# Kernel optimization log

Hardware: AMD Instinct MI355X
Metric: run time of the kernel (lower is better)

## Reference

```python
import jax, jax.numpy as jnp
import numpy as np

B, C, T = 16, 512, 1024      # batch, in_shape (channels), seq_len
H, D = 8, 64                 # num_heads, head_dim; embed = H*D == C
E = H * D
EPS = 1e-6


def setup_inputs() -> dict:
    key = jax.random.key(0)
    ks = jax.random.split(key, 10)
    s_in = 1.0 / np.sqrt(C)
    s_e = 1.0 / np.sqrt(E)
    return {
        "X": jax.random.normal(ks[0], (B, C, T), jnp.float32),
        "ln_g": jnp.ones((C,), jnp.float32),
        "ln_b": jnp.zeros((C,), jnp.float32),
        "Wq": jax.random.normal(ks[1], (C, E), jnp.float32) * s_in,
        "bq": jnp.zeros((E,), jnp.float32),
        "Wk": jax.random.normal(ks[2], (C, E), jnp.float32) * s_in,
        "bk": jnp.zeros((E,), jnp.float32),
        "Wv": jax.random.normal(ks[3], (C, E), jnp.float32) * s_in,
        "bv": jnp.zeros((E,), jnp.float32),
        "Wo": jax.random.normal(ks[4], (E, C), jnp.float32) * s_e,
        "bo": jnp.zeros((C,), jnp.float32),
    }


def reference(X, ln_g, ln_b, Wq, bq, Wk, bk, Wv, bv, Wo, bo):
    # dimshuffle: (B, C, T) -> (B, T, C)
    x = jnp.transpose(X, (0, 2, 1))
    # pre-norm LayerNorm over last dim, eps=1e-6
    mu = jnp.mean(x, axis=-1, keepdims=True)
    var = jnp.mean(jnp.square(x - mu), axis=-1, keepdims=True)
    xn = (x - mu) * jax.lax.rsqrt(var + EPS) * ln_g + ln_b
    # QKV projections, split into heads: (B, T, H, D)
    q = (xn @ Wq + bq).reshape(B, T, H, D)
    k = (xn @ Wk + bk).reshape(B, T, H, D)
    v = (xn @ Wv + bv).reshape(B, T, H, D)
    # attention: scores (B, H, T, T)
    scores = jnp.einsum("bqhd,bkhd->bhqk", q, k) / np.sqrt(D)
    w = jax.nn.softmax(scores, axis=-1)
    h = jnp.einsum("bhqk,bkhd->bqhd", w, v).reshape(B, T, E)
    out = h @ Wo + bo            # output projection (dropout=0 in eval)
    out = x + out                # residual
    return jnp.transpose(out, (0, 2, 1))  # back to (B, C, T)
```

## Files before the change

### kernel.cpp

```cpp
#include <hip/hip_runtime.h>
#include <hip/hip_bf16.h>
#include <cstdint>
#include <cstddef>

typedef __attribute__((ext_vector_type(8))) __bf16 bf16x8;
typedef __attribute__((ext_vector_type(4))) float f32x4;
typedef __attribute__((ext_vector_type(16))) float f32x16;
typedef __attribute__((ext_vector_type(4))) unsigned short u16x4;
typedef __attribute__((ext_vector_type(4))) unsigned int u32x4;
typedef unsigned int u32;

#define NB 16
#define NC 512
#define NT 1024
#define NH 8
#define ND 64
#define NE 512

__device__ __forceinline__ void gld16(void* lds, const void* g) {
  __builtin_amdgcn_global_load_lds(
      (const __attribute__((address_space(1))) u32*)g,
      (__attribute__((address_space(3))) u32*)lds, 16, 0, 0);
}

__device__ __forceinline__ unsigned short f2bf(float f) {
  __bf16 h = (__bf16)f;
  return __builtin_bit_cast(unsigned short, h);
}

__device__ __forceinline__ float ex2(float x) {
  float r; asm("v_exp_f32 %0, %1" : "=v"(r) : "v"(x)); return r;
}

__device__ __forceinline__ void pl32swap(u32& a, u32& b) {
  asm("v_permlane32_swap_b32 %0, %1" : "+v"(a), "+v"(b));
}

__global__ __launch_bounds__(256) void wt_convert4(
    const float* __restrict__ Wq, const float* __restrict__ Wk,
    const float* __restrict__ Wv, const float* __restrict__ Wo,
    __bf16* __restrict__ Wtq, __bf16* __restrict__ Wtk,
    __bf16* __restrict__ Wtv, __bf16* __restrict__ Wto)
{
  __shared__ float tile[32][33];
  const int w = blockIdx.y;
  const float* W = (w == 0) ? Wq : (w == 1) ? Wk : (w == 2) ? Wv : Wo;
  __bf16*     Wt = (w == 0) ? Wtq : (w == 1) ? Wtk : (w == 2) ? Wtv : Wto;
  const int bx = blockIdx.x & 15, by = blockIdx.x >> 4;
  const int r0 = by * 32, c0 = bx * 32;
  const int tx = threadIdx.x & 31, ty = threadIdx.x >> 5;
#pragma unroll
  for (int i = 0; i < 4; i++)
    tile[ty + i * 8][tx] = W[(size_t)(r0 + ty + i * 8) * 512 + c0 + tx];
  __syncthreads();
#pragma unroll
  for (int i = 0; i < 4; i++) {
    const int cc = ty + i * 8;
    Wt[(size_t)(c0 + cc) * 512 + r0 + tx] = (__bf16)tile[tx][cc];
  }
}

__global__ __launch_bounds__(256) void ln_kernel(
    const float* __restrict__ X, const float* __restrict__ gam,
    const float* __restrict__ bet, __bf16* __restrict__ xn)
{
  __shared__ float tile[16][513];
  __shared__ float mu_s[16], rs_s[16];
  const int b  = blockIdx.x >> 6;
  const int t0 = (blockIdx.x & 63) << 4;
  const int tid = threadIdx.x;
  const int tl = tid & 15, c0 = tid >> 4;
  const float* Xb = X + (size_t)b * NC * NT + t0;
  for (int c = c0; c < NC; c += 16)
    tile[tl][c] = Xb[(size_t)c * NT + tl];
  __syncthreads();
  const int row = tid >> 4, sub = tid & 15;
  float s = 0.f, s2 = 0.f;
  for (int c = sub; c < NC; c += 16) { const float v = tile[row][c]; s += v; s2 += v * v; }
  s += __shfl_xor(s, 1);  s2 += __shfl_xor(s2, 1);
  s += __shfl_xor(s, 2);  s2 += __shfl_xor(s2, 2);
  s += __shfl_xor(s, 4);  s2 += __shfl_xor(s2, 4);
  s += __shfl_xor(s, 8);  s2 += __shfl_xor(s2, 8);
  const float mu   = s * (1.f / NC);
  const float var  = s2 * (1.f / NC) - mu * mu;
  const float rstd = rsqrtf(var + 1e-6f);
  if (sub == 0) { mu_s[row] = mu; rs_s[row] = rstd; }
  __syncthreads();
  __bf16* xo = xn + ((size_t)b * NT + t0) * NC;
  for (int i = tid; i < 16 * NC; i += 256) {
    const int r = i >> 9, c = i & (NC - 1);
    xo[(size_t)r * NC + c] = (__bf16)((tile[r][c] - mu_s[r]) * rs_s[r] * gam[c] + bet[c]);
  }
}

__global__ __launch_bounds__(256) void gemm_qkv(
    const __bf16* __restrict__ A, const __bf16* __restrict__ Wt,
    const float* __restrict__ bq, const float* __restrict__ bk, const float* __restrict__ bv,
    __bf16* __restrict__ qb, __bf16* __restrict__ kb, __bf16* __restrict__ vtb)
{
  __shared__ __align__(16) __bf16 lA[128 * 64];
  __shared__ __align__(16) __bf16 lB[128 * 64];
  __shared__ float tb[4][16][17];
  const int tid = threadIdx.x;
  const int wv = tid >> 6, lane = tid & 63;
  const int bid = blockIdx.x;
  const int mchunk = bid / 192, rem = bid % 192;
  const int xcd = rem & 7, loc = rem >> 3;
  const int mt = mchunk * 16 + xcd * 2 + (loc / 12);
  const int nt = loc % 12;
  const int m0 = mt << 7, n0 = nt << 7;
  const int fr = lane & 15, kq = lane >> 4;
  const int wr = wv >> 1, wc = wv & 1;
  const int swz = (fr & 7) << 4;

  const int so  = wv * 1024 + lane * 16;
  const int srr = so >> 7;
  const int scb = (so & 127) ^ ((srr & 7) << 4);
  const char* Asrc = (const char*)A  + (size_t)(m0 + srr) * 1024 + scb;
  const char* Bsrc = (const char*)Wt + (size_t)(n0 + srr) * 1024 + scb;

  f32x4 acc[4][4] = {};
  for (int k0 = 0; k0 < 8; k0++) {
#pragma unroll
    for (int is = 0; is < 4; is++) {
      gld16((char*)lA + is * 4096 + wv * 1024, Asrc + k0 * 128 + (size_t)is * 32768);
      gld16((char*)lB + is * 4096 + wv * 1024, Bsrc + k0 * 128 + (size_t)is * 32768);
    }
    __syncthreads();
#pragma unroll
    for (int kk = 0; kk < 2; kk++) {
      bf16x8 af[4], bfr[4];
#pragma unroll
      for (int i = 0; i < 4; i++) {
        af[i]  = *(const bf16x8*)((const char*)lA +
                   (wr * 64 + i * 16 + fr) * 128 + ((kk * 64 + kq * 16) ^ swz));
        bfr[i] = *(const bf16x8*)((const char*)lB +
                   (wc * 64 + i * 16 + fr) * 128 + ((kk * 64 + kq * 16) ^ swz));
      }
#pragma unroll
      for (int i = 0; i < 4; i++)
#pragma unroll
        for (int j = 0; j < 4; j++)
          acc[i][j] = __builtin_amdgcn_mfma_f32_16x16x32_bf16(af[i], bfr[j], acc[i][j], 0, 0, 0);
    }
    __syncthreads();
  }

  const int wsel = n0 >> 9;
  const float* bias = (wsel == 0) ? bq : (wsel == 1) ? bk : bv;
  const float qsc = (wsel == 0) ? 0.18033688011112042f : 1.0f;
  if (wsel < 2) {
#pragma unroll
    for (int i = 0; i < 4; i++) {
#pragma unroll
      for (int j = 0; j < 4; j++) {
        const int ng = (n0 & 511) + wc * 64 + j * 16 + fr;
        const int hh = ng >> 6, dd = ng & 63;
        const float bb = bias[ng];
#pragma unroll
        for (int r = 0; r < 4; r++) {
          const int mg = m0 + wr * 64 + i * 16 + kq * 4 + r;
          const int b = mg >> 10, t = mg & 1023;
          const __bf16 h16 = (__bf16)((acc[i][j][r] + bb) * qsc);
          if (wsel == 0) qb[(((size_t)b * NH + hh) * NT + t) * ND + dd] = h16;
          else           kb[(((size_t)b * NH + hh) * NT + t) * ND + dd] = h16;
        }
      }
    }
  } else {
#pragma unroll
    for (int i = 0; i < 4; i++) {
#pragma unroll
      for (int j = 0; j < 4; j++) {
#pragma unroll
        for (int r = 0; r < 4; r++) tb[wv][kq * 4 + r][fr] = acc[i][j][r];
#pragma unroll
        for (int rr = 0; rr < 4; rr++) {
          const int cloc = kq * 4 + rr;
          const int ng = (n0 & 511) + wc * 64 + j * 16 + cloc;
          const int hh = ng >> 6, dd = ng & 63;
          const int mg = m0 + wr * 64 + i * 16 + fr;
          const int b = mg >> 10, t = mg & 1023;
          vtb[(((size_t)b * NH + hh) * ND + dd) * NT + t] =
              (__bf16)(tb[wv][fr][cloc] + bias[ng]);
        }
      }
    }
  }
}

__global__ __launch_bounds__(128, 2) void attn_kernel(
    const __bf16* __restrict__ qb, const __bf16* __restrict__ kb,
    const __bf16* __restrict__ vtb, __bf16* __restrict__ hb)
{
  __shared__ __align__(16) __bf16 lK[2][4096];
  __shared__ __align__(16) __bf16 lV[2][4096];
  const int tid = threadIdx.x, wv = tid >> 6, lane = tid & 63;
  const int l31 = lane & 31, hi = lane >> 5;
  const int swz = (l31 & 7) << 4;
  const int bid = blockIdx.x;
  const int xcd = bid & 7, idx = bid >> 3;
  const int hbp = xcd * 16 + (idx >> 3);
  const int chunk = idx & 7;
  const int b = hbp >> 3, hh = hbp & 7;
  const int q0 = chunk * 128 + wv * 64;

  const __bf16* Q = qb + ((size_t)b * NH + hh) * NT * ND;
  const char* Kc = (const char*)(kb  + ((size_t)b * NH + hh) * NT * ND);
  const char* Vc = (const char*)(vtb + ((size_t)b * NH + hh) * ND * NT);

  const int so  = wv * 1024 + lane * 16;
  const int srr = so >> 7;
  const int scb = (so & 127) ^ ((srr & 7) << 4);
  const char* Ksrc0 = Kc + (size_t)srr * 128 + scb;
  const char* Vsrc0 = Vc + (size_t)srr * 2048 + scb;

  bf16x8 qf[2][4];
#pragma unroll
  for (int qs = 0; qs < 2; qs++)
#pragma unroll
    for (int ds = 0; ds < 4; ds++)
      qf[qs][ds] = *(const bf16x8*)&Q[(size_t)(q0 + qs * 32 + l31) * ND + ds * 16 + hi * 8];

  float l_run[2] = {0.f, 0.f};
  f32x16 O[2][2] = {};
  const f32x16 zz = {};

  auto stage = [&](int nb, int kt64) {
#pragma unroll
    for (int is = 0; is < 4; is++) {
      gld16((char*)&lK[nb][0] + is * 2048 + wv * 1024,
            Ksrc0 + (size_t)kt64 * 128 + is * 2048);
      gld16((char*)&lV[nb][0] + is * 2048 + wv * 1024,
            Vsrc0 + (size_t)kt64 * 2 + is * 32768);
    }
  };

  stage(0, 0);
  stage(1, 64);

#pragma unroll 1
  for (int ti = 0; ti < 16; ti++) {
    const int cur = ti & 1;
    if (ti < 15) asm volatile("s_waitcnt vmcnt(8)" ::: "memory");
    else         asm volatile("s_waitcnt vmcnt(0)" ::: "memory");
    __builtin_amdgcn_s_barrier();
    __builtin_amdgcn_sched_barrier(0);
    const char* Kb = (const char*)&lK[cur][0];
    const char* Vb = (const char*)&lV[cur][0];

    f32x16 st[2][2];
    __builtin_amdgcn_s_setprio(1);
#pragma unroll
    for (int ks = 0; ks < 2; ks++) {
#pragma unroll
      for (int ds = 0; ds < 4; ds++) {
        const int row = ks * 32 + l31;
        const bf16x8 ka = *(const bf16x8*)
            (Kb + row * 128 + ((ds * 32 + hi * 16) ^ swz));
        if (ds == 0) {
          st[0][ks] = __builtin_amdgcn_mfma_f32_32x32x16_bf16(ka, qf[0][0], zz, 0, 0, 0);
          st[1][ks] = __builtin_amdgcn_mfma_f32_32x32x16_bf16(ka, qf[1][0], zz, 0, 0, 0);
        } else {
          st[0][ks] = __builtin_amdgcn_mfma_f32_32x32x16_bf16(ka, qf[0][ds], st[0][ks], 0, 0, 0);
          st[1][ks] = __builtin_amdgcn_mfma_f32_32x32x16_bf16(ka, qf[1][ds], st[1][ks], 0, 0, 0);
        }
      }
    }
    __builtin_amdgcn_s_setprio(0);

#pragma unroll
    for (int qs = 0; qs < 2; qs++) {
      float rs = 0.f;
      u32 pk[2][4][2];
#pragma unroll
      for (int ks = 0; ks < 2; ks++)
#pragma unroll
        for (int g = 0; g < 4; g++) {
          const float p0 = ex2(st[qs][ks][4 * g + 0]);
          const float p1 = ex2(st[qs][ks][4 * g + 1]);
          const float p2 = ex2(st[qs][ks][4 * g + 2]);
          const float p3 = ex2(st[qs][ks][4 * g + 3]);
          rs += (p0 + p1) + (p2 + p3);
          asm("v_cvt_pk_bf16_f32 %0, %1, %2" : "=v"(pk[ks][g][0]) : "v"(p0), "v"(p1));
          asm("v_cvt_pk_bf16_f32 %0, %1, %2" : "=v"(pk[ks][g][1]) : "v"(p2), "v"(p3));
        }
      l_run[qs] += rs;

      __builtin_amdgcn_s_setprio(1);
#pragma unroll
      for (int s = 0; s < 4; s++) {
        const int t = s >> 1, m = s & 1;
        u32 a0 = pk[t][2 * m][0], b0 = pk[t][2 * m + 1][0];
        u32 a1 = pk[t][2 * m][1], b1 = pk[t][2 * m + 1][1];
        pl32swap(a0, b0);
        pl32swap(a1, b1);
        u32x4 w;
        w[0] = a0; w[1] = a1; w[2] = b0; w[3] = b1;
        const bf16x8 pfrag = __builtin_bit_cast(bf16x8, w);
#pragma unroll
        for (int dsub = 0; dsub < 2; dsub++) {
          const int row = dsub * 32 + l31;
          const bf16x8 vf = *(const bf16x8*)
              (Vb + row * 128 + ((s * 32 + hi * 16) ^ swz));
          O[qs][dsub] = __builtin_amdgcn_mfma_f32_32x32x16_bf16(vf, pfrag, O[qs][dsub], 0, 0, 0);
        }
      }
      __builtin_amdgcn_s_setprio(0);
    }

    __builtin_amdgcn_s_barrier();
    __builtin_amdgcn_sched_barrier(0);
    if (ti + 2 < 16) stage(cur, (ti + 2) * 64);
  }

#pragma unroll
  for (int qs = 0; qs < 2; qs++) {
    const float lt = l_run[qs] + __shfl_xor(l_run[qs], 32);
    const float linv = 1.f / lt;
    const int t = q0 + qs * 32 + l31;
    __bf16* hrow = hb + ((size_t)b * NT + t) * NE + hh * ND;
#pragma unroll
    for (int dsub = 0; dsub < 2; dsub++)
#pragma unroll
      for (int g = 0; g < 4; g++) {
        u16x4 ov;
#pragma unroll
        for (int rr = 0; rr < 4; rr++) ov[rr] = f2bf(O[qs][dsub][4 * g + rr] * linv);
        *(u16x4*)&hrow[dsub * 32 + g * 8 + hi * 4] = ov;
      }
  }
}

__global__ __launch_bounds__(256) void gemm_out(
    const __bf16* __restrict__ A, const __bf16* __restrict__ Wt,
    const float* __restrict__ bo, const float* __restrict__ X,
    float* __restrict__ out)
{
  __shared__ __align__(16) __bf16 lA[128 * 64];
  __shared__ __align__(16) __bf16 lB[128 * 64];
  __shared__ float tb[4][16][17];
  const int tid = threadIdx.x, wv = tid >> 6, lane = tid & 63;
  const int bid = blockIdx.x;
  const int mt = ((bid >> 5) << 3) + (bid & 7);
  const int nt = (bid & 31) >> 3;
  const int m0 = mt << 7, n0 = nt << 7;
  const int fr = lane & 15, kq = lane >> 4;
  const int wr = wv >> 1, wc = wv & 1;
  const int swz = (fr & 7) << 4;

  const int so  = wv * 1024 + lane * 16;
  const int srr = so >> 7;
  const int scb = (so & 127) ^ ((srr & 7) << 4);
  const char* Asrc = (const char*)A  + (size_t)(m0 + srr) * 1024 + scb;
  const char* Bsrc = (const char*)Wt + (size_t)(n0 + srr) * 1024 + scb;

  f32x4 acc[4][4] = {};
  for (int k0 = 0; k0 < 8; k0++) {
#pragma unroll
    for (int is = 0; is < 4; is++) {
      gld16((char*)lA + is * 4096 + wv * 1024, Asrc + k0 * 128 + (size_t)is * 32768);
      gld16((char*)lB + is * 4096 + wv * 1024, Bsrc + k0 * 128 + (size_t)is * 32768);
    }
    __syncthreads();
#pragma unroll
    for (int kk = 0; kk < 2; kk++) {
      bf16x8 af[4], bfr[4];
#pragma unroll
      for (int i = 0; i < 4; i++) {
        af[i]  = *(const bf16x8*)((const char*)lA +
                   (wr * 64 + i * 16 + fr) * 128 + ((kk * 64 + kq * 16) ^ swz));
        bfr[i] = *(const bf16x8*)((const char*)lB +
                   (wc * 64 + i * 16 + fr) * 128 + ((kk * 64 + kq * 16) ^ swz));
      }
#pragma unroll
      for (int i = 0; i < 4; i++)
#pragma unroll
        for (int j = 0; j < 4; j++)
          acc[i][j] = __builtin_amdgcn_mfma_f32_16x16x32_bf16(af[i], bfr[j], acc[i][j], 0, 0, 0);
    }
    __syncthreads();
  }

#pragma unroll
  for (int i = 0; i < 4; i++) {
#pragma unroll
    for (int j = 0; j < 4; j++) {
#pragma unroll
      for (int r = 0; r < 4; r++) tb[wv][kq * 4 + r][fr] = acc[i][j][r];
#pragma unroll
      for (int rr = 0; rr < 4; rr++) {
        const int cloc = kq * 4 + rr;
        const int mg = m0 + wr * 64 + i * 16 + fr;
        const int b = mg >> 10, t = mg & 1023;
        const int c = n0 + wc * 64 + j * 16 + cloc;
        out[((size_t)b * NC + c) * NT + t] =
            tb[wv][fr][cloc] + bo[c] + X[((size_t)b * NC + c) * NT + t];
      }
    }
  }
}

extern "C" void kernel_launch(void* const* d_in, const int* in_sizes, int n_in,
                              void* d_out, int out_size, void* d_ws, size_t ws_size,
                              hipStream_t stream) {
  const float* X   = (const float*)d_in[0];
  const float* lng = (const float*)d_in[1];
  const float* lnb = (const float*)d_in[2];
  const float* Wq  = (const float*)d_in[3];
  const float* bq  = (const float*)d_in[4];
  const float* Wk  = (const float*)d_in[5];
  const float* bk  = (const float*)d_in[6];
  const float* Wv  = (const float*)d_in[7];
  const float* bv  = (const float*)d_in[8];
  const float* Wo  = (const float*)d_in[9];
  const float* bo  = (const float*)d_in[10];
  float* out = (float*)d_out;

  __bf16* wsb   = (__bf16*)d_ws;
  __bf16* Wtqkv = wsb;
  __bf16* Wot   = wsb + 786432;
  __bf16* xn    = wsb + 1048576;
  __bf16* qbuf  = wsb + 9437184;
  __bf16* kbuf  = wsb + 17825792;
  __bf16* vtbuf = wsb + 26214400;
  __bf16* hbuf  = wsb + 34603008;

  wt_convert4<<<dim3(256, 4), 256, 0, stream>>>(
      Wq, Wk, Wv, Wo, Wtqkv, Wtqkv + 262144, Wtqkv + 524288, Wot);
  ln_kernel<<<NB * (NT / 16), 256, 0, stream>>>(X, lng, lnb, xn);
  gemm_qkv<<<128 * 12, 256, 0, stream>>>(xn, Wtqkv, bq, bk, bv, qbuf, kbuf, vtbuf);
  attn_kernel<<<1024, 128, 0, stream>>>(qbuf, kbuf, vtbuf, hbuf);
  gemm_out<<<128 * 4, 256, 0, stream>>>(hbuf, Wot, bo, X, out);
}
```

Baseline: 132.6 us.

## Halve attention tile sizes: 32 queries per wave, 32-key blocks, double grid

```diff
diff --git a/kernel.cpp b/kernel.cpp
--- a/kernel.cpp
+++ b/kernel.cpp
@@ -189,147 +189,144 @@
   }
 }
 
-__global__ __launch_bounds__(128, 2) void attn_kernel(
+__global__ __launch_bounds__(128) void attn_kernel(
     const __bf16* __restrict__ qb, const __bf16* __restrict__ kb,
     const __bf16* __restrict__ vtb, __bf16* __restrict__ hb)
 {
-  __shared__ __align__(16) __bf16 lK[2][4096];
-  __shared__ __align__(16) __bf16 lV[2][4096];
+  __shared__ __align__(16) __bf16 lK[2][2048];
+  __shared__ __align__(16) __bf16 lV[2][2048];
   const int tid = threadIdx.x, wv = tid >> 6, lane = tid & 63;
   const int l31 = lane & 31, hi = lane >> 5;
   const int swz = (l31 & 7) << 4;
   const int bid = blockIdx.x;
   const int xcd = bid & 7, idx = bid >> 3;
-  const int hbp = xcd * 16 + (idx >> 3);
-  const int chunk = idx & 7;
+  const int hbp = xcd * 16 + (idx >> 4);
+  const int chunk = idx & 15;
   const int b = hbp >> 3, hh = hbp & 7;
-  const int q0 = chunk * 128 + wv * 64;
+  const int q0 = chunk * 64 + wv * 32;
 
   const __bf16* Q = qb + ((size_t)b * NH + hh) * NT * ND;
   const char* Kc = (const char*)(kb  + ((size_t)b * NH + hh) * NT * ND);
   const char* Vc = (const char*)(vtb + ((size_t)b * NH + hh) * ND * NT);
 
-  const int so  = wv * 1024 + lane * 16;
-  const int srr = so >> 7;
-  const int scb = (so & 127) ^ ((srr & 7) << 4);
-  const char* Ksrc0 = Kc + (size_t)srr * 128 + scb;
-  const char* Vsrc0 = Vc + (size_t)srr * 2048 + scb;
-
-  bf16x8 qf[2][4];
-#pragma unroll
-  for (int qs = 0; qs < 2; qs++)
-#pragma unroll
-    for (int ds = 0; ds < 4; ds++)
-      qf[qs][ds] = *(const bf16x8*)&Q[(size_t)(q0 + qs * 32 + l31) * ND + ds * 16 + hi * 8];
-
-  float l_run[2] = {0.f, 0.f};
-  f32x16 O[2][2] = {};
+  const char* Ks[2];
+  const char* Vs[2];
+#pragma unroll
+  for (int is = 0; is < 2; is++) {
+    const int o  = wv * 2048 + is * 1024 + lane * 16;
+    const int rr = o >> 7, ob = o & 127;
+    const int kcb = ob ^ ((rr & 7) << 4);
+    Ks[is] = Kc + (size_t)rr * 128 + kcb;
+    const int u = ob ^ ((rr & 7) << 4);
+    const int dsub = u >> 6, tb = u & 63;
+    Vs[is] = Vc + (size_t)(dsub * 32 + rr) * 2048 + tb;
+  }
+
+  bf16x8 qf[4];
+#pragma unroll
+  for (int ds = 0; ds < 4; ds++)
+    qf[ds] = *(const bf16x8*)&Q[(size_t)(q0 + l31) * ND + ds * 16 + hi * 8];
+
+  float l_run = 0.f;
+  f32x16 O[2] = {};
   const f32x16 zz = {};
 
-  auto stage = [&](int nb, int kt64) {
-#pragma unroll
-    for (int is = 0; is < 4; is++) {
-      gld16((char*)&lK[nb][0] + is * 2048 + wv * 1024,
-            Ksrc0 + (size_t)kt64 * 128 + is * 2048);
-      gld16((char*)&lV[nb][0] + is * 2048 + wv * 1024,
-            Vsrc0 + (size_t)kt64 * 2 + is * 32768);
+  auto stage = [&](int nb, int kt32) {
+#pragma unroll
+    for (int is = 0; is < 2; is++) {
+      gld16((char*)&lK[nb][0] + wv * 1024 + is * 512 * 2,
+            Ks[is] + (size_t)kt32 * 128);
+      gld16((char*)&lV[nb][0] + wv * 1024 + is * 512 * 2,
+            Vs[is] + (size_t)kt32 * 2);
     }
   };
 
-  stage(0, 0);
-  stage(1, 64);
+  auto stage2 = [&](int nb, int kt32) {
+#pragma unroll
+    for (int is = 0; is < 2; is++) {
+      gld16((char*)&lK[nb][0] + wv * 2048 + is * 1024,
+            Ks[is] + (size_t)kt32 * 128);
+      gld16((char*)&lV[nb][0] + wv * 2048 + is * 1024,
+            Vs[is] + (size_t)kt32 * 2);
+    }
+  };
+
+  stage2(0, 0);
+  stage2(1, 32);
 
 #pragma unroll 1
-  for (int ti = 0; ti < 16; ti++) {
+  for (int ti = 0; ti < 32; ti++) {
     const int cur = ti & 1;
-    if (ti < 15) asm volatile("s_waitcnt vmcnt(8)" ::: "memory");
+    if (ti < 31) asm volatile("s_waitcnt vmcnt(4)" ::: "memory");
     else         asm volatile("s_waitcnt vmcnt(0)" ::: "memory");
     __builtin_amdgcn_s_barrier();
     __builtin_amdgcn_sched_barrier(0);
     const char* Kb = (const char*)&lK[cur][0];
     const char* Vb = (const char*)&lV[cur][0];
 
-    f32x16 st[2][2];
+    f32x16 st;
     __builtin_amdgcn_s_setprio(1);
 #pragma unroll
-    for (int ks = 0; ks < 2; ks++) {
-#pragma unroll
-      for (int ds = 0; ds < 4; ds++) {
-        const int row = ks * 32 + l31;
-        const bf16x8 ka = *(const bf16x8*)
-            (Kb + row * 128 + ((ds * 32 + hi * 16) ^ swz));
-        if (ds == 0) {
-          st[0][ks] = __builtin_amdgcn_mfma_f32_32x32x16_bf16(ka, qf[0][0], zz, 0, 0, 0);
-          st[1][ks] = __builtin_amdgcn_mfma_f32_32x32x16_bf16(ka, qf[1][0], zz, 0, 0, 0);
-        } else {
-          st[0][ks] = __builtin_amdgcn_mfma_f32_32x32x16_bf16(ka, qf[0][ds], st[0][ks], 0, 0, 0);
-          st[1][ks] = __builtin_amdgcn_mfma_f32_32x32x16_bf16(ka, qf[1][ds], st[1][ks], 0, 0, 0);
-        }
-      }
+    for (int ds = 0; ds < 4; ds++) {
+      const bf16x8 ka = *(const bf16x8*)
+          (Kb + l31 * 128 + ((ds * 32 + hi * 16) ^ swz));
+      st = (ds == 0)
+         ? __builtin_amdgcn_mfma_f32_32x32x16_bf16(ka, qf[0], zz, 0, 0, 0)
+         : __builtin_amdgcn_mfma_f32_32x32x16_bf16(ka, qf[ds], st, 0, 0, 0);
     }
     __builtin_amdgcn_s_setprio(0);
 
-#pragma unroll
-    for (int qs = 0; qs < 2; qs++) {
-      float rs = 0.f;
-      u32 pk[2][4][2];
-#pragma unroll
-      for (int ks = 0; ks < 2; ks++)
-#pragma unroll
-        for (int g = 0; g < 4; g++) {
-          const float p0 = ex2(st[qs][ks][4 * g + 0]);
-          const float p1 = ex2(st[qs][ks][4 * g + 1]);
-          const float p2 = ex2(st[qs][ks][4 * g + 2]);
-          const float p3 = ex2(st[qs][ks][4 * g + 3]);
-          rs += (p0 + p1) + (p2 + p3);
-          asm("v_cvt_pk_bf16_f32 %0, %1, %2" : "=v"(pk[ks][g][0]) : "v"(p0), "v"(p1));
-          asm("v_cvt_pk_bf16_f32 %0, %1, %2" : "=v"(pk[ks][g][1]) : "v"(p2), "v"(p3));
-        }
-      l_run[qs] += rs;
-
-      __builtin_amdgcn_s_setprio(1);
-#pragma unroll
-      for (int s = 0; s < 4; s++) {
-        const int t = s >> 1, m = s & 1;
-        u32 a0 = pk[t][2 * m][0], b0 = pk[t][2 * m + 1][0];
-        u32 a1 = pk[t][2 * m][1], b1 = pk[t][2 * m + 1][1];
-        pl32swap(a0, b0);
-        pl32swap(a1, b1);
-        u32x4 w;
-        w[0] = a0; w[1] = a1; w[2] = b0; w[3] = b1;
-        const bf16x8 pfrag = __builtin_bit_cast(bf16x8, w);
-#pragma unroll
-        for (int dsub = 0; dsub < 2; dsub++) {
-          const int row = dsub * 32 + l31;
-          const bf16x8 vf = *(const bf16x8*)
-              (Vb + row * 128 + ((s * 32 + hi * 16) ^ swz));
-          O[qs][dsub] = __builtin_amdgcn_mfma_f32_32x32x16_bf16(vf, pfrag, O[qs][dsub], 0, 0, 0);
-        }
-      }
-      __builtin_amdgcn_s_setprio(0);
-    }
+    float rs = 0.f;
+    u32 pk[4][2];
+#pragma unroll
+    for (int g = 0; g < 4; g++) {
+      const float p0 = ex2(st[4 * g + 0]);
+      const float p1 = ex2(st[4 * g + 1]);
+      const float p2 = ex2(st[4 * g + 2]);
+      const float p3 = ex2(st[4 * g + 3]);
+      rs += (p0 + p1) + (p2 + p3);
+      asm("v_cvt_pk_bf16_f32 %0, %1, %2" : "=v"(pk[g][0]) : "v"(p0), "v"(p1));
+      asm("v_cvt_pk_bf16_f32 %0, %1, %2" : "=v"(pk[g][1]) : "v"(p2), "v"(p3));
+    }
+    l_run += rs;
+
+    __builtin_amdgcn_s_setprio(1);
+#pragma unroll
+    for (int s = 0; s < 2; s++) {
+      u32 a0 = pk[2 * s][0], b0 = pk[2 * s + 1][0];
+      u32 a1 = pk[2 * s][1], b1 = pk[2 * s + 1][1];
+      pl32swap(a0, b0);
+      pl32swap(a1, b1);
+      u32x4 w;
+      w[0] = a0; w[1] = a1; w[2] = b0; w[3] = b1;
+      const bf16x8 pfrag = __builtin_bit_cast(bf16x8, w);
+#pragma unroll
+      for (int dsub = 0; dsub < 2; dsub++) {
+        const bf16x8 vf = *(const bf16x8*)
+            (Vb + l31 * 128 + ((dsub * 64 + s * 32 + hi * 16) ^ swz));
+        O[dsub] = __builtin_amdgcn_mfma_f32_32x32x16_bf16(vf, pfrag, O[dsub], 0, 0, 0);
+      }
+    }
+    __builtin_amdgcn_s_setprio(0);
 
     __builtin_amdgcn_s_barrier();
     __builtin_amdgcn_sched_barrier(0);
-    if (ti + 2 < 16) stage(cur, (ti + 2) * 64);
-  }
-
-#pragma unroll
-  for (int qs = 0; qs < 2; qs++) {
-    const float lt = l_run[qs] + __shfl_xor(l_run[qs], 32);
-    const float linv = 1.f / lt;
-    const int t = q0 + qs * 32 + l31;
-    __bf16* hrow = hb + ((size_t)b * NT + t) * NE + hh * ND;
-#pragma unroll
-    for (int dsub = 0; dsub < 2; dsub++)
-#pragma unroll
-      for (int g = 0; g < 4; g++) {
-        u16x4 ov;
-#pragma unroll
-        for (int rr = 0; rr < 4; rr++) ov[rr] = f2bf(O[qs][dsub][4 * g + rr] * linv);
-        *(u16x4*)&hrow[dsub * 32 + g * 8 + hi * 4] = ov;
-      }
-  }
+    if (ti + 2 < 32) stage2(cur, (ti + 2) * 32);
+  }
+
+  const float lt = l_run + __shfl_xor(l_run, 32);
+  const float linv = 1.f / lt;
+  const int t = q0 + l31;
+  __bf16* hrow = hb + ((size_t)b * NT + t) * NE + hh * ND;
+#pragma unroll
+  for (int dsub = 0; dsub < 2; dsub++)
+#pragma unroll
+    for (int g = 0; g < 4; g++) {
+      u16x4 ov;
+#pragma unroll
+      for (int rr = 0; rr < 4; rr++) ov[rr] = f2bf(O[dsub][4 * g + rr] * linv);
+      *(u16x4*)&hrow[dsub * 32 + g * 8 + hi * 4] = ov;
+    }
 }
 
 __global__ __launch_bounds__(256) void gemm_out(
@@ -430,6 +427,6 @@
       Wq, Wk, Wv, Wo, Wtqkv, Wtqkv + 262144, Wtqkv + 524288, Wot);
   ln_kernel<<<NB * (NT / 16), 256, 0, stream>>>(X, lng, lnb, xn);
   gemm_qkv<<<128 * 12, 256, 0, stream>>>(xn, Wtqkv, bq, bk, bv, qbuf, kbuf, vtbuf);
-  attn_kernel<<<1024, 128, 0, stream>>>(qbuf, kbuf, vtbuf, hbuf);
+  attn_kernel<<<2048, 128, 0, stream>>>(qbuf, kbuf, vtbuf, hbuf);
   gemm_out<<<128 * 4, 256, 0, stream>>>(hbuf, Wot, bo, X, out);
 }
```

Result: slower. 143.3 us (+8.1%).

## Software-pipeline attention: overlap next QK^T with current softmax-PV using smaller KV tiles

Applied to the files above, without the earlier changes.

```diff
diff --git a/kernel.cpp b/kernel.cpp
--- a/kernel.cpp
+++ b/kernel.cpp
@@ -189,12 +189,12 @@
   }
 }
 
-__global__ __launch_bounds__(128, 2) void attn_kernel(
+__global__ __launch_bounds__(128) void attn_kernel(
     const __bf16* __restrict__ qb, const __bf16* __restrict__ kb,
     const __bf16* __restrict__ vtb, __bf16* __restrict__ hb)
 {
-  __shared__ __align__(16) __bf16 lK[2][4096];
-  __shared__ __align__(16) __bf16 lV[2][4096];
+  __shared__ __align__(16) __bf16 lK[3][2048];
+  __shared__ __align__(16) __bf16 lV[2][2048];
   const int tid = threadIdx.x, wv = tid >> 6, lane = tid & 63;
   const int l31 = lane & 31, hi = lane >> 5;
   const int swz = (l31 & 7) << 4;
@@ -209,11 +209,17 @@
   const char* Kc = (const char*)(kb  + ((size_t)b * NH + hh) * NT * ND);
   const char* Vc = (const char*)(vtb + ((size_t)b * NH + hh) * ND * NT);
 
-  const int so  = wv * 1024 + lane * 16;
-  const int srr = so >> 7;
-  const int scb = (so & 127) ^ ((srr & 7) << 4);
-  const char* Ksrc0 = Kc + (size_t)srr * 128 + scb;
-  const char* Vsrc0 = Vc + (size_t)srr * 2048 + scb;
+  const char* KsP[2];
+  const char* VsP[2];
+#pragma unroll
+  for (int is = 0; is < 2; is++) {
+    const int o  = wv * 2048 + is * 1024 + lane * 16;
+    const int rr = o >> 7, ob = o & 127;
+    const int cb = ob ^ ((rr & 7) << 4);
+    KsP[is] = Kc + (size_t)rr * 128 + cb;
+    const int dsub = cb >> 6, tb = cb & 63;
+    VsP[is] = Vc + (size_t)(dsub * 32 + rr) * 2048 + tb;
+  }
 
   bf16x8 qf[2][4];
 #pragma unroll
@@ -226,73 +232,59 @@
   f32x16 O[2][2] = {};
   const f32x16 zz = {};
 
-  auto stage = [&](int nb, int kt64) {
-#pragma unroll
-    for (int is = 0; is < 4; is++) {
-      gld16((char*)&lK[nb][0] + is * 2048 + wv * 1024,
-            Ksrc0 + (size_t)kt64 * 128 + is * 2048);
-      gld16((char*)&lV[nb][0] + is * 2048 + wv * 1024,
-            Vsrc0 + (size_t)kt64 * 2 + is * 32768);
-    }
+  auto stageK = [&](int kbuf, int kt) {
+#pragma unroll
+    for (int is = 0; is < 2; is++)
+      gld16((char*)&lK[kbuf][0] + wv * 2048 + is * 1024,
+            KsP[is] + (size_t)kt * 128);
   };
-
-  stage(0, 0);
-  stage(1, 64);
-
-#pragma unroll 1
-  for (int ti = 0; ti < 16; ti++) {
-    const int cur = ti & 1;
-    if (ti < 15) asm volatile("s_waitcnt vmcnt(8)" ::: "memory");
-    else         asm volatile("s_waitcnt vmcnt(0)" ::: "memory");
-    __builtin_amdgcn_s_barrier();
-    __builtin_amdgcn_sched_barrier(0);
-    const char* Kb = (const char*)&lK[cur][0];
-    const char* Vb = (const char*)&lV[cur][0];
-
-    f32x16 st[2][2];
+  auto stageV = [&](int vbuf, int kt) {
+#pragma unroll
+    for (int is = 0; is < 2; is++)
+      gld16((char*)&lV[vbuf][0] + wv * 2048 + is * 1024,
+            VsP[is] + (size_t)kt * 2);
+  };
+
+  auto qk = [&](f32x16 (&st)[2], int kbuf) {
+    const char* Kb = (const char*)&lK[kbuf][0];
     __builtin_amdgcn_s_setprio(1);
 #pragma unroll
-    for (int ks = 0; ks < 2; ks++) {
-#pragma unroll
-      for (int ds = 0; ds < 4; ds++) {
-        const int row = ks * 32 + l31;
-        const bf16x8 ka = *(const bf16x8*)
-            (Kb + row * 128 + ((ds * 32 + hi * 16) ^ swz));
-        if (ds == 0) {
-          st[0][ks] = __builtin_amdgcn_mfma_f32_32x32x16_bf16(ka, qf[0][0], zz, 0, 0, 0);
-          st[1][ks] = __builtin_amdgcn_mfma_f32_32x32x16_bf16(ka, qf[1][0], zz, 0, 0, 0);
-        } else {
-          st[0][ks] = __builtin_amdgcn_mfma_f32_32x32x16_bf16(ka, qf[0][ds], st[0][ks], 0, 0, 0);
-          st[1][ks] = __builtin_amdgcn_mfma_f32_32x32x16_bf16(ka, qf[1][ds], st[1][ks], 0, 0, 0);
-        }
+    for (int ds = 0; ds < 4; ds++) {
+      const bf16x8 ka = *(const bf16x8*)
+          (Kb + l31 * 128 + ((ds * 32 + hi * 16) ^ swz));
+      if (ds == 0) {
+        st[0] = __builtin_amdgcn_mfma_f32_32x32x16_bf16(ka, qf[0][0], zz, 0, 0, 0);
+        st[1] = __builtin_amdgcn_mfma_f32_32x32x16_bf16(ka, qf[1][0], zz, 0, 0, 0);
+      } else {
+        st[0] = __builtin_amdgcn_mfma_f32_32x32x16_bf16(ka, qf[0][ds], st[0], 0, 0, 0);
+        st[1] = __builtin_amdgcn_mfma_f32_32x32x16_bf16(ka, qf[1][ds], st[1], 0, 0, 0);
       }
     }
     __builtin_amdgcn_s_setprio(0);
-
+  };
+
+  auto smpv = [&](f32x16 (&st)[2], int vbuf) {
+    const char* Vb = (const char*)&lV[vbuf][0];
 #pragma unroll
     for (int qs = 0; qs < 2; qs++) {
       float rs = 0.f;
-      u32 pk[2][4][2];
-#pragma unroll
-      for (int ks = 0; ks < 2; ks++)
-#pragma unroll
-        for (int g = 0; g < 4; g++) {
-          const float p0 = ex2(st[qs][ks][4 * g + 0]);
-          const float p1 = ex2(st[qs][ks][4 * g + 1]);
-          const float p2 = ex2(st[qs][ks][4 * g + 2]);
-          const float p3 = ex2(st[qs][ks][4 * g + 3]);
-          rs += (p0 + p1) + (p2 + p3);
-          asm("v_cvt_pk_bf16_f32 %0, %1, %2" : "=v"(pk[ks][g][0]) : "v"(p0), "v"(p1));
-          asm("v_cvt_pk_bf16_f32 %0, %1, %2" : "=v"(pk[ks][g][1]) : "v"(p2), "v"(p3));
-        }
+      u32 pk[4][2];
+#pragma unroll
+      for (int g = 0; g < 4; g++) {
+        const float p0 = ex2(st[qs][4 * g + 0]);
+        const float p1 = ex2(st[qs][4 * g + 1]);
+        const float p2 = ex2(st[qs][4 * g + 2]);
+        const float p3 = ex2(st[qs][4 * g + 3]);
+        rs += (p0 + p1) + (p2 + p3);
+        asm("v_cvt_pk_bf16_f32 %0, %1, %2" : "=v"(pk[g][0]) : "v"(p0), "v"(p1));
+        asm("v_cvt_pk_bf16_f32 %0, %1, %2" : "=v"(pk[g][1]) : "v"(p2), "v"(p3));
+      }
       l_run[qs] += rs;
-
       __builtin_amdgcn_s_setprio(1);
 #pragma unroll
-      for (int s = 0; s < 4; s++) {
-        const int t = s >> 1, m = s & 1;
-        u32 a0 = pk[t][2 * m][0], b0 = pk[t][2 * m + 1][0];
-        u32 a1 = pk[t][2 * m][1], b1 = pk[t][2 * m + 1][1];
+      for (int s = 0; s < 2; s++) {
+        u32 a0 = pk[2 * s][0], b0 = pk[2 * s + 1][0];
+        u32 a1 = pk[2 * s][1], b1 = pk[2 * s + 1][1];
         pl32swap(a0, b0);
         pl32swap(a1, b1);
         u32x4 w;
@@ -300,18 +292,52 @@
         const bf16x8 pfrag = __builtin_bit_cast(bf16x8, w);
 #pragma unroll
         for (int dsub = 0; dsub < 2; dsub++) {
-          const int row = dsub * 32 + l31;
           const bf16x8 vf = *(const bf16x8*)
-              (Vb + row * 128 + ((s * 32 + hi * 16) ^ swz));
+              (Vb + l31 * 128 + ((dsub * 64 + s * 32 + hi * 16) ^ swz));
           O[qs][dsub] = __builtin_amdgcn_mfma_f32_32x32x16_bf16(vf, pfrag, O[qs][dsub], 0, 0, 0);
         }
       }
       __builtin_amdgcn_s_setprio(0);
     }
-
+  };
+
+  f32x16 stA[2], stB[2];
+
+  stageK(0, 0);
+  stageK(1, 32); stageV(0, 0);
+  stageK(2, 64); stageV(1, 32);
+  asm volatile("s_waitcnt vmcnt(8)" ::: "memory");
+  __builtin_amdgcn_s_barrier();
+  __builtin_amdgcn_sched_barrier(0);
+  qk(stA, 0);
+
+  int b0 = 0, b1 = 1, b2 = 2;
+#pragma unroll 1
+  for (int it = 0; it < 16; it++) {
+    const int te = 2 * it;
+    if (te < 30) asm volatile("s_waitcnt vmcnt(4)" ::: "memory");
+    else         asm volatile("s_waitcnt vmcnt(2)" ::: "memory");
     __builtin_amdgcn_s_barrier();
     __builtin_amdgcn_sched_barrier(0);
-    if (ti + 2 < 16) stage(cur, (ti + 2) * 64);
+    qk(stB, b1);
+    smpv(stA, 0);
+    __builtin_amdgcn_s_barrier();
+    __builtin_amdgcn_sched_barrier(0);
+    if (te <= 28) stageK(b0, (te + 3) * 32);
+    if (te <= 29) stageV(0, (te + 2) * 32);
+    const int to = te + 1;
+    if (to <= 29) asm volatile("s_waitcnt vmcnt(4)" ::: "memory");
+    else          asm volatile("s_waitcnt vmcnt(0)" ::: "memory");
+    __builtin_amdgcn_s_barrier();
+    __builtin_amdgcn_sched_barrier(0);
+    if (to < 31) qk(stA, b2);
+    smpv(stB, 1);
+    __builtin_amdgcn_s_barrier();
+    __builtin_amdgcn_sched_barrier(0);
+    if (to <= 28) stageK(b1, (to + 3) * 32);
+    if (to <= 29) stageV(1, (to + 2) * 32);
+    const int n0_ = b2, n1_ = b0, n2_ = b1;
+    b0 = n0_; b1 = n1_; b2 = n2_;
   }
 
 #pragma unroll
```

Measured after the change: 154.8 us. 1.17x slower.
